# Performance work log

Measured on AMD Instinct MI355X. Metric: run time of the kernel, lower is better.

Reference implementation:

```python
import jax, jax.numpy as jnp
import numpy as np

VOCAB = 200000   # emb_size
D = 128          # emb_dimension
B = 32768        # number of target groups
C = 8            # context window (group size in the consecutive-dedup)
K = 5            # negatives per (target, context) pair


def setup_inputs() -> dict:
    key = jax.random.key(0)
    k1, k2, k3, k4 = jax.random.split(key, 4)
    initrange = 1.0 / D
    u_weights = jax.random.uniform(k1, (VOCAB, D), minval=-initrange, maxval=initrange, dtype=jnp.float32)
    # torch inits v to 0; use small random values so the loss/grads are non-degenerate
    v_weights = jax.random.normal(k2, (VOCAB, D), dtype=jnp.float32) * 0.01
    # targets: consecutive blocks of C identical ids, adjacent blocks differ
    targets = (jnp.arange(B, dtype=jnp.int32) * 7919) % VOCAB
    pos_u = jnp.repeat(targets, C)                                   # [B*C]
    pos_v = jax.random.randint(k3, (B * C,), 0, VOCAB, dtype=jnp.int32)
    neg_v = jax.random.randint(k4, (B * C, K), 0, VOCAB, dtype=jnp.int32)
    return {"u_weights": u_weights, "v_weights": v_weights,
            "pos_u": pos_u, "pos_v": pos_v, "neg_v": neg_v,
            "context_size": C}


def reference(u_weights, v_weights, pos_u, pos_v, neg_v, context_size):
    Cc = context_size
    Bn = pos_u.shape[0] // Cc
    Dd = u_weights.shape[1]
    Kk = neg_v.shape[1]
    # dedup of consecutive identical targets -> one row per group of C
    U = u_weights[pos_u[::Cc]]                                  # [B, D]
    # group-sum of context embeddings (torch.split + per-group sum)
    V = v_weights[pos_v].reshape(Bn, Cc, Dd).sum(axis=1)        # [B, D]
    # per-group flattened negatives: [B, C*K, D]
    Nv = v_weights[neg_v.reshape(-1)].reshape(Bn, Cc * Kk, Dd)
    pos_score = jnp.clip(jnp.sum(U * V, axis=1), -10.0, 10.0)   # [B]
    pos_loss = -jax.nn.log_sigmoid(pos_score)
    neg_scores = jnp.clip(jnp.einsum('bnd,bd->bn', Nv, V), -10.0, 10.0)  # [B, C*K]
    neg_loss = -jnp.mean(jax.nn.log_sigmoid(-neg_scores), axis=1)        # [B]
    return jnp.mean(pos_loss + neg_loss)
```

## Files before the change

### kernel.cpp

```cpp
#include <hip/hip_runtime.h>

#define DCONST 128
#define CCTX   8
#define CK     40

__device__ __forceinline__ float logsig(float x) {
    float ax = fabsf(x);
    return fminf(x, 0.0f) - log1pf(__expf(-ax));
}

__global__ __launch_bounds__(256) void cbow_loss_kernel(
    const float* __restrict__ uw,
    const float* __restrict__ vw,
    const int*   __restrict__ pos_u,
    const int*   __restrict__ pos_v,
    const int*   __restrict__ neg_v,
    float*       __restrict__ out,
    int B, float invB)
{
    const int lane = threadIdx.x & 63;
    const int t    = lane & 15;
    const int g    = lane >> 4;
    const int wid    = (blockIdx.x * blockDim.x + threadIdx.x) >> 6;
    const int nwaves = (gridDim.x * blockDim.x) >> 6;

    float acc = 0.0f;

    for (int b = wid; b < B; b += nwaves) {
        const int base = b * CCTX;

        float4 Va = make_float4(0.f, 0.f, 0.f, 0.f);
        float4 Vb = make_float4(0.f, 0.f, 0.f, 0.f);
        #pragma unroll
        for (int c = 0; c < CCTX; ++c) {
            const int row = pos_v[base + c];
            const float4* p = (const float4*)(vw + (size_t)row * DCONST + t * 8);
            float4 a = p[0], b2 = p[1];
            Va.x += a.x;  Va.y += a.y;  Va.z += a.z;  Va.w += a.w;
            Vb.x += b2.x; Vb.y += b2.y; Vb.z += b2.z; Vb.w += b2.w;
        }

        const int urow = pos_u[base];
        const float4* up = (const float4*)(uw + (size_t)urow * DCONST + t * 8);
        float4 ua = up[0], ub = up[1];
        float p = ua.x * Va.x + ua.y * Va.y + ua.z * Va.z + ua.w * Va.w
                + ub.x * Vb.x + ub.y * Vb.y + ub.z * Vb.z + ub.w * Vb.w;
        p += __shfl_xor(p, 1);
        p += __shfl_xor(p, 2);
        p += __shfl_xor(p, 4);
        p += __shfl_xor(p, 8);
        float pos_score = fminf(fmaxf(p, -10.0f), 10.0f);
        float loss = -logsig(pos_score);

        float negacc = 0.0f;
        const long long nb = (long long)b * CK;
        #pragma unroll
        for (int it = 0; it < CK / 4; ++it) {
            const int row = neg_v[nb + it * 4 + g];
            const float4* q = (const float4*)(vw + (size_t)row * DCONST + t * 8);
            float4 ra = q[0], rb = q[1];
            float s = ra.x * Va.x + ra.y * Va.y + ra.z * Va.z + ra.w * Va.w
                    + rb.x * Vb.x + rb.y * Vb.y + rb.z * Vb.z + rb.w * Vb.w;
            s += __shfl_xor(s, 1);
            s += __shfl_xor(s, 2);
            s += __shfl_xor(s, 4);
            s += __shfl_xor(s, 8);
            s = fminf(fmaxf(s, -10.0f), 10.0f);
            negacc += -logsig(-s);
        }
        negacc += __shfl_xor(negacc, 16);
        negacc += __shfl_xor(negacc, 32);

        loss += negacc * (1.0f / CK);
        acc  += loss;
    }

    if (lane == 0) atomicAdd(out, acc * invB);
}

extern "C" void kernel_launch(void* const* d_in, const int* in_sizes, int n_in,
                              void* d_out, int out_size, void* d_ws, size_t ws_size,
                              hipStream_t stream) {
    const float* uw    = (const float*)d_in[0];
    const float* vw    = (const float*)d_in[1];
    const int*   pos_u = (const int*)d_in[2];
    const int*   pos_v = (const int*)d_in[3];
    const int*   neg_v = (const int*)d_in[4];
    float* out = (float*)d_out;

    const int B = in_sizes[2] / CCTX;

    hipMemsetAsync(out, 0, sizeof(float), stream);

    dim3 block(256);
    dim3 grid(2048);
    cbow_loss_kernel<<<grid, block, 0, stream>>>(uw, vw, pos_u, pos_v, neg_v,
                                                 out, B, 1.0f / (float)B);
}
```

Baseline: 397.8 us.

## Convert v_weights to bf16 in workspace and gather half-width rows

Adds a pre-pass kernel that converts the whole v embedding table to bf16 (round-to-nearest-even) in the workspace. The loss kernel then gathers 256-byte bf16 rows instead of 512-byte fp32 rows for both context and negative lookups, and accumulates in fp32. The intent is to roughly halve the random-gather traffic, which dominates this kernel. In exchange, every call pays a full streaming pass over the table (read fp32, write bf16) and loses precision in the dot products. An fp32 fallback kernel runs when the workspace is too small.

```diff
diff --git a/kernel.cpp b/kernel.cpp
--- a/kernel.cpp
+++ b/kernel.cpp
@@ -4,18 +4,48 @@
 #define CCTX   8
 #define CK     40
 
+typedef __attribute__((ext_vector_type(8))) unsigned short us8;
+typedef __attribute__((ext_vector_type(4))) float f32x4;
+
 __device__ __forceinline__ float logsig(float x) {
     float ax = fabsf(x);
     return fminf(x, 0.0f) - log1pf(__expf(-ax));
 }
 
-__global__ __launch_bounds__(256) void cbow_loss_kernel(
-    const float* __restrict__ uw,
-    const float* __restrict__ vw,
-    const int*   __restrict__ pos_u,
-    const int*   __restrict__ pos_v,
-    const int*   __restrict__ neg_v,
-    float*       __restrict__ out,
+__device__ __forceinline__ unsigned short f32_to_bf16_rne(float f) {
+    unsigned int u = __float_as_uint(f);
+    u += 0x7fffu + ((u >> 16) & 1u);
+    return (unsigned short)(u >> 16);
+}
+__device__ __forceinline__ float bf16_to_f32(unsigned short h) {
+    return __uint_as_float(((unsigned int)h) << 16);
+}
+
+__global__ __launch_bounds__(256) void convert_vw_kernel(
+    const float* __restrict__ vw, unsigned short* __restrict__ vwb, int n8)
+{
+    int idx    = blockIdx.x * blockDim.x + threadIdx.x;
+    int stride = gridDim.x * blockDim.x;
+    for (int i = idx; i < n8; i += stride) {
+        const f32x4* p = (const f32x4*)(vw + (size_t)i * 8);
+        f32x4 a = __builtin_nontemporal_load(p);
+        f32x4 b = __builtin_nontemporal_load(p + 1);
+        us8 o;
+        o[0] = f32_to_bf16_rne(a.x); o[1] = f32_to_bf16_rne(a.y);
+        o[2] = f32_to_bf16_rne(a.z); o[3] = f32_to_bf16_rne(a.w);
+        o[4] = f32_to_bf16_rne(b.x); o[5] = f32_to_bf16_rne(b.y);
+        o[6] = f32_to_bf16_rne(b.z); o[7] = f32_to_bf16_rne(b.w);
+        *(us8*)(vwb + (size_t)i * 8) = o;
+    }
+}
+
+__global__ __launch_bounds__(256) void cbow_loss_bf16_kernel(
+    const float*          __restrict__ uw,
+    const unsigned short* __restrict__ vwb,
+    const int*            __restrict__ pos_u,
+    const int*            __restrict__ pos_v,
+    const int*            __restrict__ neg_v,
+    float*                __restrict__ out,
     int B, float invB)
 {
     const int lane = threadIdx.x & 63;
@@ -29,22 +59,23 @@
     for (int b = wid; b < B; b += nwaves) {
         const int base = b * CCTX;
 
-        float4 Va = make_float4(0.f, 0.f, 0.f, 0.f);
-        float4 Vb = make_float4(0.f, 0.f, 0.f, 0.f);
+        float V0=0,V1=0,V2=0,V3=0,V4=0,V5=0,V6=0,V7=0;
         #pragma unroll
         for (int c = 0; c < CCTX; ++c) {
             const int row = pos_v[base + c];
-            const float4* p = (const float4*)(vw + (size_t)row * DCONST + t * 8);
-            float4 a = p[0], b2 = p[1];
-            Va.x += a.x;  Va.y += a.y;  Va.z += a.z;  Va.w += a.w;
-            Vb.x += b2.x; Vb.y += b2.y; Vb.z += b2.z; Vb.w += b2.w;
+            us8 r = *(const us8*)(vwb + (size_t)row * DCONST + t * 8);
+            V0 += bf16_to_f32(r[0]); V1 += bf16_to_f32(r[1]);
+            V2 += bf16_to_f32(r[2]); V3 += bf16_to_f32(r[3]);
+            V4 += bf16_to_f32(r[4]); V5 += bf16_to_f32(r[5]);
+            V6 += bf16_to_f32(r[6]); V7 += bf16_to_f32(r[7]);
         }
 
         const int urow = pos_u[base];
-        const float4* up = (const float4*)(uw + (size_t)urow * DCONST + t * 8);
-        float4 ua = up[0], ub = up[1];
-        float p = ua.x * Va.x + ua.y * Va.y + ua.z * Va.z + ua.w * Va.w
-                + ub.x * Vb.x + ub.y * Vb.y + ub.z * Vb.z + ub.w * Vb.w;
+        const f32x4* up = (const f32x4*)(uw + (size_t)urow * DCONST + t * 8);
+        f32x4 ua = __builtin_nontemporal_load(up);
+        f32x4 ub = __builtin_nontemporal_load(up + 1);
+        float p = ua.x*V0 + ua.y*V1 + ua.z*V2 + ua.w*V3
+                + ub.x*V4 + ub.y*V5 + ub.z*V6 + ub.w*V7;
         p += __shfl_xor(p, 1);
         p += __shfl_xor(p, 2);
         p += __shfl_xor(p, 4);
@@ -57,10 +88,11 @@
         #pragma unroll
         for (int it = 0; it < CK / 4; ++it) {
             const int row = neg_v[nb + it * 4 + g];
-            const float4* q = (const float4*)(vw + (size_t)row * DCONST + t * 8);
-            float4 ra = q[0], rb = q[1];
-            float s = ra.x * Va.x + ra.y * Va.y + ra.z * Va.z + ra.w * Va.w
-                    + rb.x * Vb.x + rb.y * Vb.y + rb.z * Vb.z + rb.w * Vb.w;
+            us8 r = *(const us8*)(vwb + (size_t)row * DCONST + t * 8);
+            float s = bf16_to_f32(r[0])*V0 + bf16_to_f32(r[1])*V1
+                    + bf16_to_f32(r[2])*V2 + bf16_to_f32(r[3])*V3
+                    + bf16_to_f32(r[4])*V4 + bf16_to_f32(r[5])*V5
+                    + bf16_to_f32(r[6])*V6 + bf16_to_f32(r[7])*V7;
             s += __shfl_xor(s, 1);
             s += __shfl_xor(s, 2);
             s += __shfl_xor(s, 4);
@@ -78,6 +110,57 @@
     if (lane == 0) atomicAdd(out, acc * invB);
 }
 
+__global__ __launch_bounds__(256) void cbow_loss_f32_kernel(
+    const float* __restrict__ uw, const float* __restrict__ vw,
+    const int* __restrict__ pos_u, const int* __restrict__ pos_v,
+    const int* __restrict__ neg_v, float* __restrict__ out,
+    int B, float invB)
+{
+    const int lane = threadIdx.x & 63;
+    const int t    = lane & 15;
+    const int g    = lane >> 4;
+    const int wid    = (blockIdx.x * blockDim.x + threadIdx.x) >> 6;
+    const int nwaves = (gridDim.x * blockDim.x) >> 6;
+    float acc = 0.0f;
+    for (int b = wid; b < B; b += nwaves) {
+        const int base = b * CCTX;
+        float4 Va = make_float4(0.f,0.f,0.f,0.f), Vb = make_float4(0.f,0.f,0.f,0.f);
+        #pragma unroll
+        for (int c = 0; c < CCTX; ++c) {
+            const int row = pos_v[base + c];
+            const float4* p = (const float4*)(vw + (size_t)row * DCONST + t * 8);
+            float4 a = p[0], b2 = p[1];
+            Va.x+=a.x; Va.y+=a.y; Va.z+=a.z; Va.w+=a.w;
+            Vb.x+=b2.x; Vb.y+=b2.y; Vb.z+=b2.z; Vb.w+=b2.w;
+        }
+        const int urow = pos_u[base];
+        const float4* up = (const float4*)(uw + (size_t)urow * DCONST + t * 8);
+        float4 ua = up[0], ub = up[1];
+        float p = ua.x*Va.x + ua.y*Va.y + ua.z*Va.z + ua.w*Va.w
+                + ub.x*Vb.x + ub.y*Vb.y + ub.z*Vb.z + ub.w*Vb.w;
+        p += __shfl_xor(p, 1); p += __shfl_xor(p, 2);
+        p += __shfl_xor(p, 4); p += __shfl_xor(p, 8);
+        float loss = -logsig(fminf(fmaxf(p, -10.0f), 10.0f));
+        float negacc = 0.0f;
+        const long long nb = (long long)b * CK;
+        #pragma unroll
+        for (int it = 0; it < CK / 4; ++it) {
+            const int row = neg_v[nb + it * 4 + g];
+            const float4* q = (const float4*)(vw + (size_t)row * DCONST + t * 8);
+            float4 ra = q[0], rb = q[1];
+            float s = ra.x*Va.x + ra.y*Va.y + ra.z*Va.z + ra.w*Va.w
+                    + rb.x*Vb.x + rb.y*Vb.y + rb.z*Vb.z + rb.w*Vb.w;
+            s += __shfl_xor(s, 1); s += __shfl_xor(s, 2);
+            s += __shfl_xor(s, 4); s += __shfl_xor(s, 8);
+            negacc += -logsig(-fminf(fmaxf(s, -10.0f), 10.0f));
+        }
+        negacc += __shfl_xor(negacc, 16);
+        negacc += __shfl_xor(negacc, 32);
+        acc += loss + negacc * (1.0f / CK);
+    }
+    if (lane == 0) atomicAdd(out, acc * invB);
+}
+
 extern "C" void kernel_launch(void* const* d_in, const int* in_sizes, int n_in,
                               void* d_out, int out_size, void* d_ws, size_t ws_size,
                               hipStream_t stream) {
@@ -89,11 +172,21 @@
     float* out = (float*)d_out;
 
     const int B = in_sizes[2] / CCTX;
+    const size_t vw_elems = (size_t)in_sizes[1];
+    const size_t need     = vw_elems * 2;
 
-    hipMemsetAsync(out, 0, sizeof(float), stream);
+    (void)hipMemsetAsync(out, 0, sizeof(float), stream);
 
     dim3 block(256);
     dim3 grid(2048);
-    cbow_loss_kernel<<<grid, block, 0, stream>>>(uw, vw, pos_u, pos_v, neg_v,
-                                                 out, B, 1.0f / (float)B);
+
+    if (ws_size >= need) {
+        unsigned short* vwb = (unsigned short*)d_ws;
+        convert_vw_kernel<<<grid, block, 0, stream>>>(vw, vwb, (int)(vw_elems / 8));
+        cbow_loss_bf16_kernel<<<grid, block, 0, stream>>>(uw, vwb, pos_u, pos_v,
+                                                          neg_v, out, B, 1.0f / (float)B);
+    } else {
+        cbow_loss_f32_kernel<<<grid, block, 0, stream>>>(uw, vw, pos_u, pos_v,
+                                                         neg_v, out, B, 1.0f / (float)B);
+    }
 }
```

Result: faster. 389.0 us (-2.2%).
